# Kernel tuning notes

Hardware: AMD Instinct MI355X
Metric: run time of the kernel (lower is better)

## Reference

```python
import jax, jax.numpy as jnp
import numpy as np

L, S, N, E, H = 1024, 1024, 4, 1024, 16


def setup_inputs() -> dict:
    key = jax.random.key(0)
    ks = jax.random.split(key, 7)
    return {
        "query": jax.random.normal(ks[0], (L, N, E), jnp.float32),
        "key": jax.random.normal(ks[1], (S, N, E), jnp.float32),
        "value": jax.random.normal(ks[2], (S, N, E), jnp.float32),
        "in_proj_weight": jax.random.normal(ks[3], (3 * E, E), jnp.float32) * (E ** -0.5),
        "in_proj_bias": jax.random.normal(ks[4], (3 * E,), jnp.float32) * 0.02,
        "out_proj_weight": jax.random.normal(ks[5], (E, E), jnp.float32) * (E ** -0.5),
        "out_proj_bias": jax.random.normal(ks[6], (E,), jnp.float32) * 0.02,
        "num_heads": H,
    }


def _split_heads(x, n, h, hd):
    # (T, N, E) -> (N*h, T, hd), matching torch view(T, N*h, hd).transpose(0, 1)
    t = x.shape[0]
    return jnp.transpose(x.reshape(t, n * h, hd), (1, 0, 2))


def reference(query, key, value, in_proj_weight, in_proj_bias,
              out_proj_weight, out_proj_bias, num_heads):
    tgt_len, bsz, embed_dim = query.shape
    src_len = key.shape[0]
    head_dim = embed_dim // num_heads
    scaling = float(head_dim) ** -0.5

    # packed QKV projection (torch F.linear: x @ W.T + b), sliced as in source
    q = query @ in_proj_weight[:embed_dim].T + in_proj_bias[:embed_dim]
    k = key @ in_proj_weight[embed_dim:2 * embed_dim].T + in_proj_bias[embed_dim:2 * embed_dim]
    v = value @ in_proj_weight[2 * embed_dim:].T + in_proj_bias[2 * embed_dim:]
    q = q * scaling

    q = _split_heads(q, bsz, num_heads, head_dim)  # (N*H, L, hd)
    k = _split_heads(k, bsz, num_heads, head_dim)  # (N*H, S, hd)
    v = _split_heads(v, bsz, num_heads, head_dim)  # (N*H, S, hd)

    scores = jnp.einsum('bld,bsd->bls', q, k)           # (N*H, L, S)
    attn = jax.nn.softmax(scores, axis=-1)
    ctx = jnp.einsum('bls,bsd->bld', attn, v)           # (N*H, L, hd)

    # (N*H, L, hd) -> (L, N, E)
    ctx = jnp.transpose(ctx, (1, 0, 2)).reshape(tgt_len, bsz, embed_dim)
    attn_output = ctx @ out_proj_weight.T + out_proj_bias

    # need_weights=True path: average over heads -> (N, L, S)
    attn_weights = attn.reshape(bsz, num_heads, tgt_len, src_len).sum(axis=1) / num_heads
    return attn_output, attn_weights
```

## Files before the change

kernel.cpp:

```cpp
#include <hip/hip_runtime.h>

typedef unsigned short u16;
typedef __attribute__((ext_vector_type(8))) short short8;
typedef __attribute__((ext_vector_type(4))) float f32x4;

__device__ __forceinline__ u16 f2bf(float f) {
  unsigned int i = __float_as_uint(f);
  i += 0x7fffu + ((i >> 16) & 1u);
  return (u16)(i >> 16);
}

__device__ __forceinline__ short8 cvt8(const float* p) {
  float4 a = ((const float4*)p)[0];
  float4 b = ((const float4*)p)[1];
  short8 r;
  r[0] = (short)f2bf(a.x); r[1] = (short)f2bf(a.y);
  r[2] = (short)f2bf(a.z); r[3] = (short)f2bf(a.w);
  r[4] = (short)f2bf(b.x); r[5] = (short)f2bf(b.y);
  r[6] = (short)f2bf(b.z); r[7] = (short)f2bf(b.w);
  return r;
}

__global__ __launch_bounds__(256) void convert_bf16(
    const float* __restrict__ q, const float* __restrict__ k,
    const float* __restrict__ v, const float* __restrict__ Wi,
    const float* __restrict__ Wo,
    u16* __restrict__ qb, u16* __restrict__ kb, u16* __restrict__ vb,
    u16* __restrict__ Wib, u16* __restrict__ Wob)
{
  const float* src; u16* dst; int len8;
  switch (blockIdx.y) {
    case 0:  src = q;  dst = qb;  len8 = 524288; break;
    case 1:  src = k;  dst = kb;  len8 = 524288; break;
    case 2:  src = v;  dst = vb;  len8 = 524288; break;
    case 3:  src = Wi; dst = Wib; len8 = 393216; break;
    default: src = Wo; dst = Wob; len8 = 131072; break;
  }
  int stride = gridDim.x * 256;
  for (int i = blockIdx.x * 256 + threadIdx.x; i < len8; i += stride)
    *(short8*)(dst + (size_t)i * 8) = cvt8(src + (size_t)i * 8);
}

__global__ __launch_bounds__(256) void qkv_gemm(
    const u16* __restrict__ qb, const u16* __restrict__ kb,
    const u16* __restrict__ vb, const u16* __restrict__ W,
    const float* __restrict__ bias,
    u16* __restrict__ qh, u16* __restrict__ kh, u16* __restrict__ vt)
{
  __shared__ __align__(16) u16 As[128 * 40];
  __shared__ __align__(16) u16 Bs[128 * 40];

  const int tid  = threadIdx.x;
  const int wave = tid >> 6;
  const int lane = tid & 63;
  const int r    = lane & 15;
  const int q4   = lane >> 4;
  const int wm   = wave >> 1;
  const int wn   = wave & 1;

  const int jt = blockIdx.x;
  const int mt = blockIdx.y;
  const int src = jt >> 3;
  const u16* X = (src == 0) ? qb : (src == 1) ? kb : vb;
  const int m0 = mt * 128;
  const int j0 = jt * 128;

  const int trow = tid >> 2;
  const int tcol = (tid & 3) * 8;

  f32x4 acc[4][4];
  #pragma unroll
  for (int a = 0; a < 4; ++a)
    #pragma unroll
    for (int b = 0; b < 4; ++b)
      acc[a][b] = (f32x4){0.f, 0.f, 0.f, 0.f};

  for (int kk = 0; kk < 1024; kk += 32) {
    short8 a0 = *(const short8*)(X + (size_t)(m0 + trow) * 1024 + kk + tcol);
    short8 a1 = *(const short8*)(X + (size_t)(m0 + 64 + trow) * 1024 + kk + tcol);
    short8 b0 = *(const short8*)(W + (size_t)(j0 + trow) * 1024 + kk + tcol);
    short8 b1 = *(const short8*)(W + (size_t)(j0 + 64 + trow) * 1024 + kk + tcol);
    __syncthreads();
    *(short8*)(As + trow * 40 + tcol) = a0;
    *(short8*)(As + (64 + trow) * 40 + tcol) = a1;
    *(short8*)(Bs + trow * 40 + tcol) = b0;
    *(short8*)(Bs + (64 + trow) * 40 + tcol) = b1;
    __syncthreads();

    const u16* Ab = As + (wm * 64) * 40;
    const u16* Bb = Bs + (wn * 64) * 40;
    short8 af[4], bf[4];
    #pragma unroll
    for (int mi = 0; mi < 4; ++mi)
      af[mi] = *(const short8*)(Ab + (mi * 16 + r) * 40 + q4 * 8);
    #pragma unroll
    for (int ji = 0; ji < 4; ++ji)
      bf[ji] = *(const short8*)(Bb + (ji * 16 + r) * 40 + q4 * 8);
    #pragma unroll
    for (int mi = 0; mi < 4; ++mi)
      #pragma unroll
      for (int ji = 0; ji < 4; ++ji)
        acc[mi][ji] = __builtin_amdgcn_mfma_f32_16x16x32_bf16(af[mi], bf[ji], acc[mi][ji], 0, 0, 0);
  }

  #pragma unroll
  for (int mi = 0; mi < 4; ++mi) {
    #pragma unroll
    for (int ji = 0; ji < 4; ++ji) {
      #pragma unroll
      for (int rr = 0; rr < 4; ++rr) {
        int m = m0 + wm * 64 + mi * 16 + q4 * 4 + rr;
        int j = j0 + wn * 64 + ji * 16 + r;
        float v = acc[mi][ji][rr] + bias[j];
        int t = m >> 2, n = m & 3;
        int jj = j & 1023;
        int h = jj >> 6, d = jj & 63;
        int bb = n * 16 + h;
        if (src == 0)
          qh[(size_t)bb * 65536 + (size_t)t * 64 + d] = f2bf(v * 0.125f);
        else if (src == 1)
          kh[(size_t)bb * 65536 + (size_t)t * 64 + d] = f2bf(v);
        else
          vt[(size_t)bb * 65536 + (size_t)d * 1024 + t] = f2bf(v);
      }
    }
  }
}

__global__ __launch_bounds__(256) void attn_ctx_mfma(
    const u16* __restrict__ qh, const u16* __restrict__ kh,
    const u16* __restrict__ vt, u16* __restrict__ ctx,
    float* __restrict__ Zbuf)
{
  __shared__ __align__(16) u16 Ks[2][4096];
  __shared__ __align__(16) u16 Vs[2][4096];
  __shared__ __align__(16) u16 Pl[4][1024];

  const int tid = threadIdx.x;
  const int wv = tid >> 6, lane = tid & 63, r = lane & 15, q4 = lane >> 4;
  const int b  = blockIdx.y;
  const int lw = blockIdx.x * 64 + wv * 16;
  const int n = b >> 4, h = b & 15;

  const u16* qbase = qh + (size_t)b * 65536;
  const char* kc = (const char*)(kh + (size_t)b * 65536);
  const char* vc = (const char*)(vt + (size_t)b * 65536);
  u16* P = Pl[wv];

  const int ls  = lane >> 3;
  const int swzb = ((lane & 7) ^ ls) << 4;
  const int iw  = wv * 2;
  const size_t klo = (size_t)iw * 1024 + (size_t)ls * 128 + swzb;
  const size_t vlo = (size_t)iw * 16384 + (size_t)ls * 2048 + swzb;

  const int rsw = r & 7;
  const int c0 = (q4 ^ rsw) << 3;
  const int c1 = ((q4 ^ rsw) ^ 4) << 3;

  short8 aq0 = *(const short8*)(qbase + (size_t)(lw + r) * 64 + q4 * 8);
  short8 aq1 = *(const short8*)(qbase + (size_t)(lw + r) * 64 + 32 + q4 * 8);

  f32x4 oc[4];
  #pragma unroll
  for (int ji = 0; ji < 4; ++ji) oc[ji] = (f32x4){0.f, 0.f, 0.f, 0.f};
  float z[4] = {0.f, 0.f, 0.f, 0.f};

  {
    const char* kp = kc + klo;
    const char* vp = vc + vlo;
    u16* kd = &Ks[0][iw * 512];
    u16* vd = &Vs[0][iw * 512];
    __builtin_amdgcn_global_load_lds(kp,          kd,       16, 0, 0);
    __builtin_amdgcn_global_load_lds(kp + 1024,   kd + 512, 16, 0, 0);
    __builtin_amdgcn_global_load_lds(vp,          vd,       16, 0, 0);
    __builtin_amdgcn_global_load_lds(vp + 16384,  vd + 512, 16, 0, 0);
  }

  for (int it = 0; it < 16; ++it) {
    const int cur = it & 1;
    __syncthreads();
    const u16* Kb = Ks[cur];
    const u16* Vb = Vs[cur];

    f32x4 sc[4];
    #pragma unroll
    for (int ji = 0; ji < 4; ++ji) {
      const int row = (ji * 16 + r) * 64;
      short8 bk0 = *(const short8*)(Kb + row + c0);
      short8 bk1 = *(const short8*)(Kb + row + c1);
      f32x4 t = (f32x4){0.f, 0.f, 0.f, 0.f};
      t = __builtin_amdgcn_mfma_f32_16x16x32_bf16(aq0, bk0, t, 0, 0, 0);
      t = __builtin_amdgcn_mfma_f32_16x16x32_bf16(aq1, bk1, t, 0, 0, 0);
      sc[ji] = t;
    }

    if (it < 15) {
      const char* kp = kc + (size_t)(it + 1) * 8192 + klo;
      const char* vp = vc + (size_t)(it + 1) * 128  + vlo;
      u16* kd = &Ks[cur ^ 1][iw * 512];
      u16* vd = &Vs[cur ^ 1][iw * 512];
      __builtin_amdgcn_global_load_lds(kp,          kd,       16, 0, 0);
      __builtin_amdgcn_global_load_lds(kp + 1024,   kd + 512, 16, 0, 0);
      __builtin_amdgcn_global_load_lds(vp,          vd,       16, 0, 0);
      __builtin_amdgcn_global_load_lds(vp + 16384,  vd + 512, 16, 0, 0);
    }

    #pragma unroll
    for (int ji = 0; ji < 4; ++ji) {
      const int cw = ji * 2 + (r >> 3);
      #pragma unroll
      for (int rr = 0; rr < 4; ++rr) {
        float e = __expf(sc[ji][rr]);
        z[rr] += e;
        const int row = q4 * 4 + rr;
        P[row * 64 + ((cw ^ (row & 7)) << 3) + (r & 7)] = f2bf(e);
      }
    }
    asm volatile("s_waitcnt lgkmcnt(0)" ::: "memory");
    short8 ap0 = *(const short8*)(P + r * 64 + c0);
    short8 ap1 = *(const short8*)(P + r * 64 + c1);
    #pragma unroll
    for (int ji = 0; ji < 4; ++ji) {
      const int row = (ji * 16 + r) * 64;
      short8 bv0 = *(const short8*)(Vb + row + c0);
      short8 bv1 = *(const short8*)(Vb + row + c1);
      oc[ji] = __builtin_amdgcn_mfma_f32_16x16x32_bf16(ap0, bv0, oc[ji], 0, 0, 0);
      oc[ji] = __builtin_amdgcn_mfma_f32_16x16x32_bf16(ap1, bv1, oc[ji], 0, 0, 0);
    }
  }

  #pragma unroll
  for (int rr = 0; rr < 4; ++rr) {
    float zz = z[rr];
    zz += __shfl_xor(zz, 1);
    zz += __shfl_xor(zz, 2);
    zz += __shfl_xor(zz, 4);
    zz += __shfl_xor(zz, 8);
    z[rr] = zz;
  }

  #pragma unroll
  for (int rr = 0; rr < 4; ++rr) {
    float inv = 1.0f / z[rr];
    int l = lw + q4 * 4 + rr;
    u16* crow = ctx + ((size_t)l * 4 + n) * 1024 + h * 64;
    #pragma unroll
    for (int ji = 0; ji < 4; ++ji)
      crow[ji * 16 + r] = f2bf(oc[ji][rr] * inv);
    if (r == 0) Zbuf[(size_t)b * 1024 + l] = z[rr];
  }
}

__global__ __launch_bounds__(256) void attn_w_mfma(
    const u16* __restrict__ qh, const u16* __restrict__ kh,
    const float* __restrict__ Zbuf, float* __restrict__ out_w)
{
  __shared__ __align__(16) u16 Kw[2][4096];
  __shared__ float invZ[16][64];

  const int tid = threadIdx.x;
  const int wv = tid >> 6, lane = tid & 63, r = lane & 15, q4 = lane >> 4;
  const int lt = blockIdx.x;
  const int st = blockIdx.y;
  const int n  = blockIdx.z;
  const int l0 = lt * 64;
  const int s0 = st * 64;
  const int lw = l0 + wv * 16;

  const char* khc = (const char*)kh + (size_t)n * 2097152;

  const int ls  = lane >> 3;
  const int swzb = ((lane & 7) ^ ls) << 4;
  const int iw  = wv * 2;
  const size_t klo = (size_t)s0 * 128 + (size_t)iw * 1024 + (size_t)ls * 128 + swzb;

  const int rsw = r & 7;
  const int c0 = (q4 ^ rsw) << 3;
  const int c1 = ((q4 ^ rsw) ^ 4) << 3;

  for (int i = tid; i < 1024; i += 256) {
    int hh = i >> 6, row = i & 63;
    invZ[hh][row] = 1.0f / (Zbuf[(size_t)(n * 16 + hh) * 1024 + l0 + row] * 16.0f);
  }

  {
    const char* kp = khc + klo;
    u16* kd = &Kw[0][iw * 512];
    __builtin_amdgcn_global_load_lds(kp,        kd,       16, 0, 0);
    __builtin_amdgcn_global_load_lds(kp + 1024, kd + 512, 16, 0, 0);
  }
  const u16* q0 = qh + (size_t)(n * 16) * 65536;
  short8 aqc0 = *(const short8*)(q0 + (size_t)(lw + r) * 64 + q4 * 8);
  short8 aqc1 = *(const short8*)(q0 + (size_t)(lw + r) * 64 + 32 + q4 * 8);

  f32x4 wacc[4];
  #pragma unroll
  for (int ji = 0; ji < 4; ++ji) wacc[ji] = (f32x4){0.f, 0.f, 0.f, 0.f};

  for (int hh = 0; hh < 16; ++hh) {
    const int cur = hh & 1;
    __syncthreads();
    if (hh < 15) {
      const char* kp = khc + (size_t)(hh + 1) * 131072 + klo;
      u16* kd = &Kw[cur ^ 1][iw * 512];
      __builtin_amdgcn_global_load_lds(kp,        kd,       16, 0, 0);
      __builtin_amdgcn_global_load_lds(kp + 1024, kd + 512, 16, 0, 0);
    }
    const int hn = (hh < 15) ? hh + 1 : hh;
    const u16* qn = qh + (size_t)(n * 16 + hn) * 65536;
    short8 an0 = *(const short8*)(qn + (size_t)(lw + r) * 64 + q4 * 8);
    short8 an1 = *(const short8*)(qn + (size_t)(lw + r) * 64 + 32 + q4 * 8);

    const u16* Kb = Kw[cur];
    f32x4 sc[4];
    #pragma unroll
    for (int ji = 0; ji < 4; ++ji) {
      const int row = (ji * 16 + r) * 64;
      short8 bk0 = *(const short8*)(Kb + row + c0);
      short8 bk1 = *(const short8*)(Kb + row + c1);
      f32x4 t = (f32x4){0.f, 0.f, 0.f, 0.f};
      t = __builtin_amdgcn_mfma_f32_16x16x32_bf16(aqc0, bk0, t, 0, 0, 0);
      t = __builtin_amdgcn_mfma_f32_16x16x32_bf16(aqc1, bk1, t, 0, 0, 0);
      sc[ji] = t;
    }
    #pragma unroll
    for (int rr = 0; rr < 4; ++rr) {
      float iv = invZ[hh][wv * 16 + q4 * 4 + rr];
      #pragma unroll
      for (int ji = 0; ji < 4; ++ji)
        wacc[ji][rr] += __expf(sc[ji][rr]) * iv;
    }
    aqc0 = an0; aqc1 = an1;
  }

  #pragma unroll
  for (int ji = 0; ji < 4; ++ji)
    #pragma unroll
    for (int rr = 0; rr < 4; ++rr) {
      int row = lw + q4 * 4 + rr;
      int col = s0 + ji * 16 + r;
      out_w[(size_t)n * 1048576 + (size_t)row * 1024 + col] = wacc[ji][rr];
    }
}

__global__ __launch_bounds__(256) void out_gemm(
    const u16* __restrict__ ctx, const u16* __restrict__ W,
    const float* __restrict__ bias, float* __restrict__ out)
{
  __shared__ __align__(16) u16 As[128 * 40];
  __shared__ __align__(16) u16 Bs[128 * 40];

  const int tid  = threadIdx.x;
  const int wave = tid >> 6;
  const int lane = tid & 63;
  const int r    = lane & 15;
  const int q4   = lane >> 4;
  const int wm   = wave >> 1;
  const int wn   = wave & 1;

  const int j0 = blockIdx.x * 128;
  const int m0 = blockIdx.y * 128;

  const int trow = tid >> 2;
  const int tcol = (tid & 3) * 8;

  f32x4 acc[4][4];
  #pragma unroll
  for (int a = 0; a < 4; ++a)
    #pragma unroll
    for (int b = 0; b < 4; ++b)
      acc[a][b] = (f32x4){0.f, 0.f, 0.f, 0.f};

  for (int kk = 0; kk < 1024; kk += 32) {
    short8 a0 = *(const short8*)(ctx + (size_t)(m0 + trow) * 1024 + kk + tcol);
    short8 a1 = *(const short8*)(ctx + (size_t)(m0 + 64 + trow) * 1024 + kk + tcol);
    short8 b0 = *(const short8*)(W + (size_t)(j0 + trow) * 1024 + kk + tcol);
    short8 b1 = *(const short8*)(W + (size_t)(j0 + 64 + trow) * 1024 + kk + tcol);
    __syncthreads();
    *(short8*)(As + trow * 40 + tcol) = a0;
    *(short8*)(As + (64 + trow) * 40 + tcol) = a1;
    *(short8*)(Bs + trow * 40 + tcol) = b0;
    *(short8*)(Bs + (64 + trow) * 40 + tcol) = b1;
    __syncthreads();

    const u16* Ab = As + (wm * 64) * 40;
    const u16* Bb = Bs + (wn * 64) * 40;
    short8 af[4], bf[4];
    #pragma unroll
    for (int mi = 0; mi < 4; ++mi)
      af[mi] = *(const short8*)(Ab + (mi * 16 + r) * 40 + q4 * 8);
    #pragma unroll
    for (int ji = 0; ji < 4; ++ji)
      bf[ji] = *(const short8*)(Bb + (ji * 16 + r) * 40 + q4 * 8);
    #pragma unroll
    for (int mi = 0; mi < 4; ++mi)
      #pragma unroll
      for (int ji = 0; ji < 4; ++ji)
        acc[mi][ji] = __builtin_amdgcn_mfma_f32_16x16x32_bf16(af[mi], bf[ji], acc[mi][ji], 0, 0, 0);
  }

  #pragma unroll
  for (int mi = 0; mi < 4; ++mi) {
    #pragma unroll
    for (int ji = 0; ji < 4; ++ji) {
      #pragma unroll
      for (int rr = 0; rr < 4; ++rr) {
        int m = m0 + wm * 64 + mi * 16 + q4 * 4 + rr;
        int j = j0 + wn * 64 + ji * 16 + r;
        out[(size_t)m * 1024 + j] = acc[mi][ji][rr] + bias[j];
      }
    }
  }
}

extern "C" void kernel_launch(void* const* d_in, const int* in_sizes, int n_in,
                              void* d_out, int out_size, void* d_ws, size_t ws_size,
                              hipStream_t stream) {
  const float* query = (const float*)d_in[0];
  const float* key   = (const float*)d_in[1];
  const float* value = (const float*)d_in[2];
  const float* W_in  = (const float*)d_in[3];
  const float* b_in  = (const float*)d_in[4];
  const float* W_out = (const float*)d_in[5];
  const float* b_out = (const float*)d_in[6];
  float* out = (float*)d_out;

  u16* qb  = (u16*)d_ws;
  u16* kb  = qb  + (size_t)4194304;
  u16* vb  = kb  + (size_t)4194304;
  u16* Wib = vb  + (size_t)4194304;
  u16* Wob = Wib + (size_t)3145728;
  u16* qh  = Wob + (size_t)1048576;
  u16* kh  = qh  + (size_t)4194304;
  u16* vt  = kh  + (size_t)4194304;
  u16* ctx = vt  + (size_t)4194304;
  float* Zbuf = (float*)(ctx + (size_t)4194304);

  convert_bf16<<<dim3(512, 5), 256, 0, stream>>>(query, key, value, W_in, W_out,
                                                 qb, kb, vb, Wib, Wob);
  qkv_gemm<<<dim3(24, 32), 256, 0, stream>>>(qb, kb, vb, Wib, b_in, qh, kh, vt);
  attn_ctx_mfma<<<dim3(16, 64), 256, 0, stream>>>(qh, kh, vt, ctx, Zbuf);
  attn_w_mfma<<<dim3(16, 16, 4), 256, 0, stream>>>(qh, kh, Zbuf, out + (size_t)4194304);
  out_gemm<<<dim3(8, 32), 256, 0, stream>>>(ctx, Wob, b_out, out);
}
```

Measured before the change: 249.1 us.

## Use direct global-to-LDS loads with XOR swizzle and block remap in projection GEMMs

Both projection GEMMs now stage tiles with global_load_lds straight into a 64-wide XOR-swizzled LDS layout, using a 64-element K step instead of 32. This halves the number of barriers and avoids the register round-trip. Block indices are remapped so that neighbouring blocks share operand tiles, for better L2 reuse. The output GEMM switches to 128x64 tiles with twice as many blocks to fill more CUs, at the cost of less reuse per block.

```diff
diff --git a/kernel.cpp b/kernel.cpp
--- a/kernel.cpp
+++ b/kernel.cpp
@@ -47,8 +47,8 @@
     const float* __restrict__ bias,
     u16* __restrict__ qh, u16* __restrict__ kh, u16* __restrict__ vt)
 {
-  __shared__ __align__(16) u16 As[128 * 40];
-  __shared__ __align__(16) u16 Bs[128 * 40];
+  __shared__ __align__(16) u16 As[128 * 64];
+  __shared__ __align__(16) u16 Bs[128 * 64];
 
   const int tid  = threadIdx.x;
   const int wave = tid >> 6;
@@ -58,15 +58,19 @@
   const int wm   = wave >> 1;
   const int wn   = wave & 1;
 
-  const int jt = blockIdx.x;
-  const int mt = blockIdx.y;
-  const int src = jt >> 3;
+  const int orig = blockIdx.y * 24 + blockIdx.x;
+  const int nid  = (orig & 7) * 96 + (orig >> 3);
+  const int mt   = nid / 24;
+  const int jt   = nid - mt * 24;
+  const int src  = jt >> 3;
   const u16* X = (src == 0) ? qb : (src == 1) ? kb : vb;
   const int m0 = mt * 128;
   const int j0 = jt * 128;
 
-  const int trow = tid >> 2;
-  const int tcol = (tid & 3) * 8;
+  const int ls   = lane >> 3;
+  const int swzb = ((lane & 7) ^ ls) << 4;
+  const char* Xc = (const char*)X;
+  const char* Wc = (const char*)W;
 
   f32x4 acc[4][4];
   #pragma unroll
@@ -75,32 +79,40 @@
     for (int b = 0; b < 4; ++b)
       acc[a][b] = (f32x4){0.f, 0.f, 0.f, 0.f};
 
-  for (int kk = 0; kk < 1024; kk += 32) {
-    short8 a0 = *(const short8*)(X + (size_t)(m0 + trow) * 1024 + kk + tcol);
-    short8 a1 = *(const short8*)(X + (size_t)(m0 + 64 + trow) * 1024 + kk + tcol);
-    short8 b0 = *(const short8*)(W + (size_t)(j0 + trow) * 1024 + kk + tcol);
-    short8 b1 = *(const short8*)(W + (size_t)(j0 + 64 + trow) * 1024 + kk + tcol);
-    __syncthreads();
-    *(short8*)(As + trow * 40 + tcol) = a0;
-    *(short8*)(As + (64 + trow) * 40 + tcol) = a1;
-    *(short8*)(Bs + trow * 40 + tcol) = b0;
-    *(short8*)(Bs + (64 + trow) * 40 + tcol) = b1;
-    __syncthreads();
-
-    const u16* Ab = As + (wm * 64) * 40;
-    const u16* Bb = Bs + (wn * 64) * 40;
-    short8 af[4], bf[4];
-    #pragma unroll
-    for (int mi = 0; mi < 4; ++mi)
-      af[mi] = *(const short8*)(Ab + (mi * 16 + r) * 40 + q4 * 8);
-    #pragma unroll
-    for (int ji = 0; ji < 4; ++ji)
-      bf[ji] = *(const short8*)(Bb + (ji * 16 + r) * 40 + q4 * 8);
-    #pragma unroll
-    for (int mi = 0; mi < 4; ++mi)
-      #pragma unroll
-      for (int ji = 0; ji < 4; ++ji)
-        acc[mi][ji] = __builtin_amdgcn_mfma_f32_16x16x32_bf16(af[mi], bf[ji], acc[mi][ji], 0, 0, 0);
+  for (int kt = 0; kt < 16; ++kt) {
+    const int kb2 = kt * 128;
+    __syncthreads();
+    #pragma unroll
+    for (int i = 0; i < 4; ++i) {
+      const int row = wave * 32 + i * 8 + ls;
+      __builtin_amdgcn_global_load_lds(
+          (const u16*)(Xc + (size_t)(m0 + row) * 2048 + kb2 + swzb),
+          As + (wave * 4 + i) * 512, 16, 0, 0);
+      __builtin_amdgcn_global_load_lds(
+          (const u16*)(Wc + (size_t)(j0 + row) * 2048 + kb2 + swzb),
+          Bs + (wave * 4 + i) * 512, 16, 0, 0);
+    }
+    __syncthreads();
+
+    #pragma unroll
+    for (int ks = 0; ks < 2; ++ks) {
+      short8 af[4], bf[4];
+      #pragma unroll
+      for (int mi = 0; mi < 4; ++mi) {
+        const int row = wm * 64 + mi * 16 + r;
+        af[mi] = *(const short8*)(As + row * 64 + ((((ks << 2) | q4) ^ (r & 7)) << 3));
+      }
+      #pragma unroll
+      for (int ji = 0; ji < 4; ++ji) {
+        const int row = wn * 64 + ji * 16 + r;
+        bf[ji] = *(const short8*)(Bs + row * 64 + ((((ks << 2) | q4) ^ (r & 7)) << 3));
+      }
+      #pragma unroll
+      for (int mi = 0; mi < 4; ++mi)
+        #pragma unroll
+        for (int ji = 0; ji < 4; ++ji)
+          acc[mi][ji] = __builtin_amdgcn_mfma_f32_16x16x32_bf16(af[mi], bf[ji], acc[mi][ji], 0, 0, 0);
+    }
   }
 
   #pragma unroll
@@ -347,8 +359,8 @@
     const u16* __restrict__ ctx, const u16* __restrict__ W,
     const float* __restrict__ bias, float* __restrict__ out)
 {
-  __shared__ __align__(16) u16 As[128 * 40];
-  __shared__ __align__(16) u16 Bs[128 * 40];
+  __shared__ __align__(16) u16 As[128 * 64];
+  __shared__ __align__(16) u16 Bs[64 * 64];
 
   const int tid  = threadIdx.x;
   const int wave = tid >> 6;
@@ -358,55 +370,73 @@
   const int wm   = wave >> 1;
   const int wn   = wave & 1;
 
-  const int j0 = blockIdx.x * 128;
-  const int m0 = blockIdx.y * 128;
-
-  const int trow = tid >> 2;
-  const int tcol = (tid & 3) * 8;
-
-  f32x4 acc[4][4];
+  const int orig = blockIdx.y * 16 + blockIdx.x;
+  const int nid  = (orig & 7) * 64 + (orig >> 3);
+  const int mt   = nid >> 4;
+  const int jt   = nid & 15;
+  const int m0 = mt * 128;
+  const int j0 = jt * 64;
+
+  const int ls   = lane >> 3;
+  const int swzb = ((lane & 7) ^ ls) << 4;
+  const char* Ac = (const char*)ctx;
+  const char* Wc = (const char*)W;
+
+  f32x4 acc[4][2];
   #pragma unroll
   for (int a = 0; a < 4; ++a)
     #pragma unroll
-    for (int b = 0; b < 4; ++b)
+    for (int b = 0; b < 2; ++b)
       acc[a][b] = (f32x4){0.f, 0.f, 0.f, 0.f};
 
-  for (int kk = 0; kk < 1024; kk += 32) {
-    short8 a0 = *(const short8*)(ctx + (size_t)(m0 + trow) * 1024 + kk + tcol);
-    short8 a1 = *(const short8*)(ctx + (size_t)(m0 + 64 + trow) * 1024 + kk + tcol);
-    short8 b0 = *(const short8*)(W + (size_t)(j0 + trow) * 1024 + kk + tcol);
-    short8 b1 = *(const short8*)(W + (size_t)(j0 + 64 + trow) * 1024 + kk + tcol);
-    __syncthreads();
-    *(short8*)(As + trow * 40 + tcol) = a0;
-    *(short8*)(As + (64 + trow) * 40 + tcol) = a1;
-    *(short8*)(Bs + trow * 40 + tcol) = b0;
-    *(short8*)(Bs + (64 + trow) * 40 + tcol) = b1;
-    __syncthreads();
-
-    const u16* Ab = As + (wm * 64) * 40;
-    const u16* Bb = Bs + (wn * 64) * 40;
-    short8 af[4], bf[4];
-    #pragma unroll
-    for (int mi = 0; mi < 4; ++mi)
-      af[mi] = *(const short8*)(Ab + (mi * 16 + r) * 40 + q4 * 8);
-    #pragma unroll
-    for (int ji = 0; ji < 4; ++ji)
-      bf[ji] = *(const short8*)(Bb + (ji * 16 + r) * 40 + q4 * 8);
-    #pragma unroll
-    for (int mi = 0; mi < 4; ++mi)
-      #pragma unroll
-      for (int ji = 0; ji < 4; ++ji)
-        acc[mi][ji] = __builtin_amdgcn_mfma_f32_16x16x32_bf16(af[mi], bf[ji], acc[mi][ji], 0, 0, 0);
+  for (int kt = 0; kt < 16; ++kt) {
+    const int kb2 = kt * 128;
+    __syncthreads();
+    #pragma unroll
+    for (int i = 0; i < 4; ++i) {
+      const int row = wave * 32 + i * 8 + ls;
+      __builtin_amdgcn_global_load_lds(
+          (const u16*)(Ac + (size_t)(m0 + row) * 2048 + kb2 + swzb),
+          As + (wave * 4 + i) * 512, 16, 0, 0);
+    }
+    #pragma unroll
+    for (int i = 0; i < 2; ++i) {
+      const int row = wave * 16 + i * 8 + ls;
+      __builtin_amdgcn_global_load_lds(
+          (const u16*)(Wc + (size_t)(j0 + row) * 2048 + kb2 + swzb),
+          Bs + (wave * 2 + i) * 512, 16, 0, 0);
+    }
+    __syncthreads();
+
+    #pragma unroll
+    for (int ks = 0; ks < 2; ++ks) {
+      short8 af[4], bf[2];
+      #pragma unroll
+      for (int mi = 0; mi < 4; ++mi) {
+        const int row = wm * 64 + mi * 16 + r;
+        af[mi] = *(const short8*)(As + row * 64 + ((((ks << 2) | q4) ^ (r & 7)) << 3));
+      }
+      #pragma unroll
+      for (int ji = 0; ji < 2; ++ji) {
+        const int row = wn * 32 + ji * 16 + r;
+        bf[ji] = *(const short8*)(Bs + row * 64 + ((((ks << 2) | q4) ^ (r & 7)) << 3));
+      }
+      #pragma unroll
+      for (int mi = 0; mi < 4; ++mi)
+        #pragma unroll
+        for (int ji = 0; ji < 2; ++ji)
+          acc[mi][ji] = __builtin_amdgcn_mfma_f32_16x16x32_bf16(af[mi], bf[ji], acc[mi][ji], 0, 0, 0);
+    }
   }
 
   #pragma unroll
   for (int mi = 0; mi < 4; ++mi) {
     #pragma unroll
-    for (int ji = 0; ji < 4; ++ji) {
+    for (int ji = 0; ji < 2; ++ji) {
       #pragma unroll
       for (int rr = 0; rr < 4; ++rr) {
         int m = m0 + wm * 64 + mi * 16 + q4 * 4 + rr;
-        int j = j0 + wn * 64 + ji * 16 + r;
+        int j = j0 + wn * 32 + ji * 16 + r;
         out[(size_t)m * 1024 + j] = acc[mi][ji][rr] + bias[j];
       }
     }
@@ -441,5 +471,5 @@
   qkv_gemm<<<dim3(24, 32), 256, 0, stream>>>(qb, kb, vb, Wib, b_in, qh, kh, vt);
   attn_ctx_mfma<<<dim3(16, 64), 256, 0, stream>>>(qh, kh, vt, ctx, Zbuf);
   attn_w_mfma<<<dim3(16, 16, 4), 256, 0, stream>>>(qh, kh, Zbuf, out + (size_t)4194304);
-  out_gemm<<<dim3(8, 32), 256, 0, stream>>>(ctx, Wob, b_out, out);
-}
+  out_gemm<<<dim3(16, 32), 256, 0, stream>>>(ctx, Wob, b_out, out);
+}
```

Result: no change. 246.1 us (-1.2%).
